# Kernel optimization log

Hardware: AMD Instinct MI355X
Metric: run time of the kernel (lower is better)

The kernel has to match this reference:

```python
import jax, jax.numpy as jnp
import numpy as np
from jax import lax

B, CIN, HW = 4, 3, 256      # batch, image channels, image size
HID = 128                   # hidden_size
EMB_D = 64                  # embedding_dim == encoder output channels
K = 1024                    # num_embeddings
L = 2                       # num encoder/decoder layers (1 resblock each)


def _conv(x, w, b, stride, pad):
    y = lax.conv_general_dilated(x, w, (stride, stride), ((pad, pad), (pad, pad)),
                                 dimension_numbers=('NCHW', 'OIHW', 'NCHW'))
    return y + b[None, :, None, None]


def _bn(x):
    # BatchNorm2d in training mode: batch stats over (N,H,W), affine at init (gamma=1, beta=0)
    m = x.mean((0, 2, 3), keepdims=True)
    v = x.var((0, 2, 3), keepdims=True)
    return (x - m) * lax.rsqrt(v + 1e-5)


def _resblock(x, w1, b1, w2, b2):
    y = jax.nn.relu(_bn(_conv(x, w1, b1, 1, 1)))
    y = _bn(_conv(y, w2, b2, 1, 1))
    return jax.nn.relu(y + x)


def _conv_t(x, w, b):
    # torch ConvTranspose2d(k=4, s=2, p=1); w in torch layout (I, O, 4, 4)
    wf = jnp.flip(w, (2, 3)).transpose(1, 0, 2, 3)  # (O, I, 4, 4)
    y = lax.conv_general_dilated(x, wf, (1, 1), ((2, 2), (2, 2)), lhs_dilation=(2, 2),
                                 dimension_numbers=('NCHW', 'OIHW', 'NCHW'))
    return y + b[None, :, None, None]


def _vqvae(x, enc_in_w, enc_in_b, enc_res_w1, enc_res_b1, enc_res_w2, enc_res_b2,
           enc_down_w, enc_down_b, enc_out_w, enc_out_b,
           dec_in_w, dec_in_b, dec_res_w1, dec_res_b1, dec_res_w2, dec_res_b2,
           dec_up_w, dec_up_b, dec_out_w, dec_out_b, codebook):
    sg = lax.stop_gradient
    # ---- encoder ----
    h = _conv(x, enc_in_w, enc_in_b, 1, 0)
    for i in range(L):
        h = _resblock(h, enc_res_w1[i], enc_res_b1[i], enc_res_w2[i], enc_res_b2[i])
        h = jax.nn.relu(_conv(h, enc_down_w[i], enc_down_b[i], 2, 1))
    z = _conv(h, enc_out_w, enc_out_b, 1, 0)  # (B, C, H/4, W/4)
    # ---- vector quantize ----
    Bz, C, Hl, Wl = z.shape
    zf = z.transpose(0, 2, 3, 1).reshape(-1, C)  # (N, C)
    # ||z - e||^2 expanded; same argmin as the (N,K,C) form without materializing it
    d = (zf * zf).sum(1, keepdims=True) - 2.0 * (zf @ codebook.T) + (codebook * codebook).sum(1)[None, :]
    idx = jnp.argmin(d, axis=1)  # (N,)
    z_q = codebook[idx].reshape(Bz, Hl, Wl, C).transpose(0, 3, 1, 2)
    z_q_st = z_q + sg(z - z_q)  # as in source: forward value == z, grads flow to codebook
    # ---- decoder ----
    h = _conv(z_q_st, dec_in_w, dec_in_b, 1, 0)
    for i in range(L):
        h = _resblock(h, dec_res_w1[i], dec_res_b1[i], dec_res_w2[i], dec_res_b2[i])
        h = jax.nn.relu(_conv_t(h, dec_up_w[i], dec_up_b[i]))
    recon = jax.nn.sigmoid(_conv(h, dec_out_w, dec_out_b, 1, 0))
    # ---- losses ----
    commit = jnp.mean((z - sg(z_q_st)) ** 2)
    cb_l = jnp.mean((sg(z) - z_q_st) ** 2)
    counts = jnp.zeros((K,), jnp.float32).at[idx].add(1.0)
    p = counts + 1e-6
    p = p / p.sum()
    ent = -(p * jnp.log(p)).sum()
    loss = commit + cb_l - ent
    return recon, loss, idx.reshape(Bz, Hl, Wl)


def setup_inputs() -> dict:
    key = jax.random.key(0)
    ks = iter(jax.random.split(key, 40))
    def w(shape, fan_in):
        return jax.random.normal(next(ks), shape, jnp.float32) * np.float32((2.0 / fan_in) ** 0.5)
    z128 = lambda *s: jnp.zeros(s, jnp.float32)
    return {
        'x': jax.random.uniform(next(ks), (B, CIN, HW, HW), jnp.float32),
        'enc_in_w': w((HID, CIN, 1, 1), CIN), 'enc_in_b': z128(HID),
        'enc_res_w1': w((L, HID, HID, 3, 3), HID * 9), 'enc_res_b1': z128(L, HID),
        'enc_res_w2': w((L, HID, HID, 3, 3), HID * 9), 'enc_res_b2': z128(L, HID),
        'enc_down_w': w((L, HID, HID, 4, 4), HID * 16), 'enc_down_b': z128(L, HID),
        'enc_out_w': w((EMB_D, HID, 1, 1), HID), 'enc_out_b': z128(EMB_D),
        'dec_in_w': w((HID, EMB_D, 1, 1), EMB_D), 'dec_in_b': z128(HID),
        'dec_res_w1': w((L, HID, HID, 3, 3), HID * 9), 'dec_res_b1': z128(L, HID),
        'dec_res_w2': w((L, HID, HID, 3, 3), HID * 9), 'dec_res_b2': z128(L, HID),
        'dec_up_w': w((L, HID, HID, 4, 4), HID * 16), 'dec_up_b': z128(L, HID),  # (I,O,4,4) torch layout
        'dec_out_w': w((CIN, HID, 1, 1), HID), 'dec_out_b': z128(CIN),
        'codebook': jax.random.normal(next(ks), (K, EMB_D), jnp.float32) * np.float32((2.0 / (K + EMB_D)) ** 0.5),
    }


def reference(x, enc_in_w, enc_in_b, enc_res_w1, enc_res_b1, enc_res_w2, enc_res_b2,
              enc_down_w, enc_down_b, enc_out_w, enc_out_b,
              dec_in_w, dec_in_b, dec_res_w1, dec_res_b1, dec_res_w2, dec_res_b2,
              dec_up_w, dec_up_b, dec_out_w, dec_out_b, codebook):
    return _vqvae(x, enc_in_w, enc_in_b, enc_res_w1, enc_res_b1, enc_res_w2, enc_res_b2,
                  enc_down_w, enc_down_b, enc_out_w, enc_out_b,
                  dec_in_w, dec_in_b, dec_res_w1, dec_res_b1, dec_res_w2, dec_res_b2,
                  dec_up_w, dec_up_b, dec_out_w, dec_out_b, codebook)
```

## Files before the change

### kernel.cpp

```cpp
#include <hip/hip_runtime.h>
#include <math.h>


#define RE_SIZE 786432

typedef float f32x4 __attribute__((ext_vector_type(4)));
typedef short bf16x8 __attribute__((ext_vector_type(8)));
typedef short bf16x4 __attribute__((ext_vector_type(4)));

__device__ __forceinline__ unsigned short f2bf(float f) {
  unsigned u = __float_as_uint(f);
  return (unsigned short)((u + 0x7fffu + ((u >> 16) & 1u)) >> 16);
}
__device__ __forceinline__ float bf2f(unsigned short h) {
  return __uint_as_float(((unsigned)h) << 16);
}
__device__ __forceinline__ void split3(float v, unsigned short& a,
                                       unsigned short& b, unsigned short& c) {
  a = f2bf(v); float r = v - bf2f(a);
  b = f2bf(r); r -= bf2f(b);
  c = f2bf(r);
}

__global__ __launch_bounds__(256) void weff_kernel(
    const float* __restrict__ w3, const float* __restrict__ ew,
    const float* __restrict__ eb, unsigned short* __restrict__ f0,
    unsigned short* __restrict__ f1, unsigned short* __restrict__ f2) {
  int id = blockIdx.x * 256 + threadIdx.x;
  int j = id & 7, lane = (id >> 3) & 63, mt = (id >> 9) & 7, kc = id >> 12;
  int co = mt * 16 + (lane & 15);
  int q = lane >> 4;
  int k = kc * 32 + q * 8 + j;
  int t = k >> 2, c = k & 3;
  float v = 0.f;
  if (t <= 8) {
    double acc = 0.0;
    for (int ci = 0; ci < 128; ++ci) {
      double wv = (double)w3[((long)co * 128 + ci) * 9 + t];
      double xv = (c < 3) ? (double)ew[ci * 3 + c] : (double)eb[ci];
      acc += wv * xv;
    }
    v = (float)acc;
  }
  unsigned short a, b, cc; split3(v, a, b, cc);
  f0[id] = a; f1[id] = b; f2[id] = cc;
}

__global__ __launch_bounds__(256) void conv36_mfma_kernel(
    const float* __restrict__ xin, const unsigned short* __restrict__ f0,
    const unsigned short* __restrict__ f1, const unsigned short* __restrict__ f2,
    const float* __restrict__ bias, float* __restrict__ out, int H, int W) {
  __shared__ __align__(16) unsigned short s_x[3][720];
  int tid = threadIdx.x, wv = tid >> 6, lane = tid & 63;
  int q = lane >> 4, c15 = lane & 15;
  int tilesX = W >> 4;
  int tx0 = (blockIdx.x % tilesX) << 4;
  int ty0 = (blockIdx.x / tilesX) << 3;
  int n = blockIdx.z;
  long HWl = (long)H * W;
  long ibase = (long)n * 128 * HWl;
  long xbase = (long)n * 3 * HWl;
  f32x4 acc[2][8];
#pragma unroll
  for (int a = 0; a < 2; ++a)
#pragma unroll
    for (int b = 0; b < 8; ++b) acc[a][b] = (f32x4){0.f, 0.f, 0.f, 0.f};

  for (int l = tid; l < 180; l += 256) {
    int y = l / 18, x = l % 18;
    int gy = ty0 + y - 1, gx = tx0 + x - 1;
    float v[4] = {0.f, 0.f, 0.f, 0.f};
    if ((unsigned)gy < (unsigned)H && (unsigned)gx < (unsigned)W) {
      const float* xp = xin + xbase + (long)gy * W + gx;
      v[0] = xp[0]; v[1] = xp[HWl]; v[2] = xp[2 * HWl]; v[3] = 1.f;
    }
    bf16x4 s0, s1, s2;
#pragma unroll
    for (int c = 0; c < 4; ++c) {
      unsigned short h0, h1, h2; split3(v[c], h0, h1, h2);
      s0[c] = (short)h0; s1[c] = (short)h1; s2[c] = (short)h2;
    }
    *(bf16x4*)(s_x[0] + l * 4) = s0;
    *(bf16x4*)(s_x[1] + l * 4) = s1;
    *(bf16x4*)(s_x[2] + l * 4) = s2;
  }
  __syncthreads();

#pragma unroll
  for (int kc = 0; kc < 2; ++kc) {
    bf16x8 a0[2], a1[2], a2[2];
#pragma unroll
// ... 3 lines not shown
      a1[m] = ((const bf16x8*)f1)[fi];
      a2[m] = ((const bf16x8*)f2)[fi];
    }
    int ta = kc * 8 + 2 * q; if (ta > 8) ta = 8;
    int tb = ta + 1;         if (tb > 8) tb = 8;
    int pa_d = (ta / 3) * 18 + ta % 3;
    int pb_d = (tb / 3) * 18 + tb % 3;
#pragma unroll
    for (int nn = 0; nn < 8; ++nn) {
      int pa = (nn * 18 + c15 + pa_d) * 4;
      int pb = (nn * 18 + c15 + pb_d) * 4;
      bf16x8 b0, b1v, b2;
      bf16x4 lo, hi;
      lo = *(const bf16x4*)(s_x[0] + pa); hi = *(const bf16x4*)(s_x[0] + pb);
#pragma unroll
      for (int i = 0; i < 4; ++i) { b0[i] = lo[i]; b0[4 + i] = hi[i]; }
      lo = *(const bf16x4*)(s_x[1] + pa); hi = *(const bf16x4*)(s_x[1] + pb);
#pragma unroll
      for (int i = 0; i < 4; ++i) { b1v[i] = lo[i]; b1v[4 + i] = hi[i]; }
      lo = *(const bf16x4*)(s_x[2] + pa); hi = *(const bf16x4*)(s_x[2] + pb);
#pragma unroll
      for (int i = 0; i < 4; ++i) { b2[i] = lo[i]; b2[4 + i] = hi[i]; }
#pragma unroll
      for (int m = 0; m < 2; ++m) {
        acc[m][nn] = __builtin_amdgcn_mfma_f32_16x16x32_bf16(a0[m], b0, acc[m][nn], 0, 0, 0);
        acc[m][nn] = __builtin_amdgcn_mfma_f32_16x16x32_bf16(a0[m], b1v, acc[m][nn], 0, 0, 0);
        acc[m][nn] = __builtin_amdgcn_mfma_f32_16x16x32_bf16(a1[m], b0, acc[m][nn], 0, 0, 0);
        acc[m][nn] = __builtin_amdgcn_mfma_f32_16x16x32_bf16(a0[m], b2, acc[m][nn], 0, 0, 0);
        acc[m][nn] = __builtin_amdgcn_mfma_f32_16x16x32_bf16(a1[m], b1v, acc[m][nn], 0, 0, 0);
        acc[m][nn] = __builtin_amdgcn_mfma_f32_16x16x32_bf16(a2[m], b0, acc[m][nn], 0, 0, 0);
      }
    }
  }
#pragma unroll
  for (int mt2 = 0; mt2 < 2; ++mt2) {
    int co0 = (wv * 2 + mt2) * 16 + q * 4;
#pragma unroll
    for (int nn = 0; nn < 8; ++nn) {
      long pxoff = ibase + (long)(ty0 + nn) * W + tx0 + c15;
#pragma unroll
      for (int r = 0; r < 4; ++r)
        out[pxoff + (long)(co0 + r) * HWl] = acc[mt2][nn][r] + bias[co0 + r];
    }
  }
}

__global__ __launch_bounds__(256) void wsplit_kernel(
    const float* __restrict__ w, unsigned short* __restrict__ w0,
    unsigned short* __restrict__ w1, unsigned short* __restrict__ w2) {
  int id = blockIdx.x * 256 + threadIdx.x;
  int j = id & 7, lane = (id >> 3) & 63, rest = id >> 9;
  int mt = rest & 7, rest2 = rest >> 3;
  int tap = rest2 % 9, cc = rest2 / 9;
  int co = mt * 16 + (lane & 15);
  int ci = cc * 32 + (lane >> 4) * 8 + j;
  float v = w[((long)co * 128 + ci) * 9 + tap];
  unsigned short a, b, c; split3(v, a, b, c);
  w0[id] = a; w1[id] = b; w2[id] = c;
}

__global__ __launch_bounds__(256) void wsplit4_kernel(
    const float* __restrict__ w, unsigned short* __restrict__ w0,
    unsigned short* __restrict__ w1, unsigned short* __restrict__ w2) {
  int id = blockIdx.x * 256 + threadIdx.x;
  int j = id & 7, lane = (id >> 3) & 63;
  int mt = (id >> 9) & 7, pair = (id >> 12) & 7, cc = id >> 15;
  int q = lane >> 4;
  int tap = pair * 2 + (q >> 1);
  int ky = tap >> 2, kx = tap & 3;
  int co = mt * 16 + (lane & 15);
  int ci = cc * 16 + (q & 1) * 8 + j;
  float v = w[((long)co * 128 + ci) * 16 + ky * 4 + kx];
  unsigned short a, b, c; split3(v, a, b, c);
  w0[id] = a; w1[id] = b; w2[id] = c;
}

__global__ __launch_bounds__(256) void wsplitT_kernel(
    const float* __restrict__ w, unsigned short* __restrict__ w0,
    unsigned short* __restrict__ w1) {
  int id = blockIdx.x * 256 + threadIdx.x;
  int jj = id & 7, lane = (id >> 3) & 63;
  int mt = (id >> 9) & 7, j = (id >> 12) & 3, cls = (id >> 14) & 3, cc = id >> 16;
  int py = cls >> 1, px = cls & 1, jy = j >> 1, jx = j & 1;
  int ky = py ? (jy ? 2 : 0) : (jy ? 3 : 1);
  int kx = px ? (jx ? 2 : 0) : (jx ? 3 : 1);
  int co = mt * 16 + (lane & 15);
  int ci = cc * 32 + (lane >> 4) * 8 + jj;
  float v = w[((long)ci * 128 + co) * 16 + ky * 4 + kx];
  unsigned short h = f2bf(v);
  w0[id] = h;
  w1[id] = f2bf(v - bf2f(h));
}

template<int IMODE, int SPLIT>
__global__ __launch_bounds__(256) void conv3x3_mfma_kernel(
    const float* __restrict__ in, const unsigned short* __restrict__ w0s,
    const unsigned short* __restrict__ w1s, const unsigned short* __restrict__ w2s,
    const float* __restrict__ bias, float* __restrict__ out, int H, int W,
    const float2* __restrict__ mr, const float* __restrict__ xin,
    const float* __restrict__ w1, const float* __restrict__ b1) {
  __shared__ __align__(16) unsigned short s_x[SPLIT][5760];
  int tid = threadIdx.x, wv = tid >> 6, lane = tid & 63;
  int q = lane >> 4, c15 = lane & 15;
  int tilesX = W >> 4;
  int tx0 = (blockIdx.x % tilesX) << 4;
  int ty0 = (blockIdx.x / tilesX) << 3;
  int n = blockIdx.z;
  long HWl = (long)H * W;
  long ibase = (long)n * 128 * HWl;
  f32x4 acc[2][8];
#pragma unroll
  for (int a = 0; a < 2; ++a)
#pragma unroll
    for (int b = 0; b < 8; ++b) acc[a][b] = (f32x4){0.f, 0.f, 0.f, 0.f};

  for (int cc = 0; cc < 4; ++cc) {
    __syncthreads();
    for (int l = tid; l < 720; l += 256) {
      int cig = l / 180, px = l % 180;
      int y = px / 18, x = px % 18;
      int gy = ty0 + y - 1, gx = tx0 + x - 1;
      float v[8];
      if ((unsigned)gy < (unsigned)H && (unsigned)gx < (unsigned)W) {
        if (IMODE == 2) {
          const float* xp = xin + (long)n * 3 * HWl + (long)gy * W + gx;
          float x0 = xp[0], x1 = xp[HWl], x2 = xp[2 * HWl];
#pragma unroll
          for (int c = 0; c < 8; ++c) {
            int ci = cc * 32 + cig * 8 + c;
            v[c] = fmaf(w1[ci * 3 + 0], x0,
                   fmaf(w1[ci * 3 + 1], x1,
                   fmaf(w1[ci * 3 + 2], x2, b1[ci])));
          }
        } else {
          const float* ip = in + ibase + (long)(cc * 32 + cig * 8) * HWl
                            + (long)gy * W + gx;
#pragma unroll
          for (int c = 0; c < 8; ++c) v[c] = ip[(long)c * HWl];
          if (IMODE == 1) {
#pragma unroll
            for (int c = 0; c < 8; ++c) {
              float2 s = mr[cc * 32 + cig * 8 + c];
              v[c] = fmaxf((v[c] - s.x) * s.y, 0.f);
            }
          }
        }
      } else {
#pragma unroll
        for (int c = 0; c < 8; ++c) v[c] = 0.f;
      }
      bf16x8 sv[SPLIT];
#pragma unroll
      for (int c = 0; c < 8; ++c) {
        unsigned short h0 = f2bf(v[c]); float r = v[c] - bf2f(h0);
        unsigned short h1 = f2bf(r);
        sv[0][c] = (short)h0; sv[1][c] = (short)h1;
        if (SPLIT == 3) { r -= bf2f(h1); sv[2][c] = (short)f2bf(r); }
      }
#pragma unroll
      for (int s = 0; s < SPLIT; ++s) *(bf16x8*)(s_x[s] + l * 8) = sv[s];
    }
    __syncthreads();

    for (int tap = 0; tap < 9; ++tap) {
      int dy = tap / 3, dx = tap % 3;
      long fbase = (long)((cc * 9 + tap) * 8) * 64;
      bf16x8 a0[2], a1[2], a2[2];
#pragma unroll
      for (int m = 0; m < 2; ++m) {
        long fi = fbase + (2 * wv + m) * 64 + lane;
        a0[m] = ((const bf16x8*)w0s)[fi];
        a1[m] = ((const bf16x8*)w1s)[fi];
        if (SPLIT == 3) a2[m] = ((const bf16x8*)w2s)[fi];
      }
      int xoff = (q * 180 + dy * 18 + c15 + dx) * 8;
#pragma unroll
      for (int nn = 0; nn < 8; ++nn) {
        bf16x8 b0 = *(const bf16x8*)(s_x[0] + xoff + nn * 144);
        bf16x8 b1v = *(const bf16x8*)(s_x[1] + xoff + nn * 144);
#pragma unroll
        for (int m = 0; m < 2; ++m) {
          acc[m][nn] = __builtin_amdgcn_mfma_f32_16x16x32_bf16(a0[m], b0, acc[m][nn], 0, 0, 0);
          acc[m][nn] = __builtin_amdgcn_mfma_f32_16x16x32_bf16(a0[m], b1v, acc[m][nn], 0, 0, 0);
          acc[m][nn] = __builtin_amdgcn_mfma_f32_16x16x32_bf16(a1[m], b0, acc[m][nn], 0, 0, 0);
        }
        if (SPLIT == 3) {
          bf16x8 b2 = *(const bf16x8*)(s_x[2] + xoff + nn * 144);
#pragma unroll
          for (int m = 0; m < 2; ++m) {
            acc[m][nn] = __builtin_amdgcn_mfma_f32_16x16x32_bf16(a0[m], b2, acc[m][nn], 0, 0, 0);
            acc[m][nn] = __builtin_amdgcn_mfma_f32_16x16x32_bf16(a1[m], b1v, acc[m][nn], 0, 0, 0);
            acc[m][nn] = __builtin_amdgcn_mfma_f32_16x16x32_bf16(a2[m], b0, acc[m][nn], 0, 0, 0);
          }
        }
      }
    }
  }
#pragma unroll
  for (int mt2 = 0; mt2 < 2; ++mt2) {
    int co0 = (wv * 2 + mt2) * 16 + q * 4;
#pragma unroll
    for (int nn = 0; nn < 8; ++nn) {
      long pxoff = ibase + (long)(ty0 + nn) * W + tx0 + c15;
#pragma unroll
      for (int r = 0; r < 4; ++r)
        out[pxoff + (long)(co0 + r) * HWl] = acc[mt2][nn][r] + bias[co0 + r];
    }
  }
}

__global__ __launch_bounds__(256) void down_mfma_kernel(
    const float* __restrict__ in, const unsigned short* __restrict__ w0s,
    const unsigned short* __restrict__ w1s, const unsigned short* __restrict__ w2s,
    const float* __restrict__ bias, float* __restrict__ out, int Hin, int Win) {
  __shared__ __align__(16) unsigned short s_x[3][9792];
  int tid = threadIdx.x, wv = tid >> 6, lane = tid & 63;
  int q = lane >> 4, c15 = lane & 15;
  int Hout = Hin >> 1, Wout = Win >> 1;
  int tilesX = Wout >> 4;
  int tx0 = (blockIdx.x % tilesX) << 4;
  int ty0 = (blockIdx.x / tilesX) << 3;
  int n = blockIdx.z;
  long HWin = (long)Hin * Win, HWout = (long)Hout * Wout;
  long ibase = (long)n * 128 * HWin, obase = (long)n * 128 * HWout;
  f32x4 acc[2][8];
#pragma unroll
  for (int a = 0; a < 2; ++a)
#pragma unroll
    for (int b = 0; b < 8; ++b) acc[a][b] = (f32x4){0.f, 0.f, 0.f, 0.f};

  for (int cc = 0; cc < 8; ++cc) {
    __syncthreads();
    for (int l = tid; l < 1224; l += 256) {
      int cig = l / 612, rem = l % 612;
      int g = rem / 153, p = rem % 153;
      int py = p / 17, px_ = p % 17;
      int gy = g >> 1, gx = g & 1;
      int iy = 2 * (ty0 + py - gy) + gy;
      int ix = 2 * (tx0 + px_ - gx) + gx;
      float v[8];
      if ((unsigned)iy < (unsigned)Hin && (unsigned)ix < (unsigned)Win) {
        const float* ip = in + ibase + (long)(cc * 16 + cig * 8) * HWin
                          + (long)iy * Win + ix;
#pragma unroll
        for (int c = 0; c < 8; ++c) v[c] = ip[(long)c * HWin];
      } else {
#pragma unroll
        for (int c = 0; c < 8; ++c) v[c] = 0.f;
      }
      bf16x8 s0, s1, s2;
#pragma unroll
      for (int c = 0; c < 8; ++c) {
        unsigned short h0, h1, h2; split3(v[c], h0, h1, h2);
        s0[c] = (short)h0; s1[c] = (short)h1; s2[c] = (short)h2;
      }
      *(bf16x8*)(s_x[0] + l * 8) = s0;
      *(bf16x8*)(s_x[1] + l * 8) = s1;
      *(bf16x8*)(s_x[2] + l * 8) = s2;
    }
    __syncthreads();

    for (int pr = 0; pr < 8; ++pr) {
      long fbase = (long)((cc * 8 + pr) * 8) * 64;
      bf16x8 a0[2], a1[2], a2[2];
#pragma unroll
      for (int m = 0; m < 2; ++m) {
        long fi = fbase + (2 * wv + m) * 64 + lane;
        a0[m] = ((const bf16x8*)w0s)[fi];
        a1[m] = ((const bf16x8*)w1s)[fi];
        a2[m] = ((const bf16x8*)w2s)[fi];
      }
      int tap = pr * 2 + (q >> 1);
      int ky = tap >> 2, kx = tap & 3;
      int gy = (ky + 1) & 1, gx = (kx + 1) & 1;
      int dy = (ky == 0) ? -1 : ((ky == 3) ? 1 : 0);
      int dx = (kx == 0) ? -1 : ((kx == 3) ? 1 : 0);
      int g = gy * 2 + gx, cig = q & 1;
      int xoff = ((cig * 4 + g) * 153 + (dy + gy) * 17 + (c15 + dx + gx)) * 8;
#pragma unroll
      for (int nn = 0; nn < 8; ++nn) {
        bf16x8 b0 = *(const bf16x8*)(s_x[0] + xoff + nn * 136);
        bf16x8 b1v = *(const bf16x8*)(s_x[1] + xoff + nn * 136);
        bf16x8 b2 = *(const bf16x8*)(s_x[2] + xoff + nn * 136);
#pragma unroll
        for (int m = 0; m < 2; ++m) {
          acc[m][nn] = __builtin_amdgcn_mfma_f32_16x16x32_bf16(a0[m], b0, acc[m][nn], 0, 0, 0);
          acc[m][nn] = __builtin_amdgcn_mfma_f32_16x16x32_bf16(a0[m], b1v, acc[m][nn], 0, 0, 0);
          acc[m][nn] = __builtin_amdgcn_mfma_f32_16x16x32_bf16(a1[m], b0, acc[m][nn], 0, 0, 0);
          acc[m][nn] = __builtin_amdgcn_mfma_f32_16x16x32_bf16(a0[m], b2, acc[m][nn], 0, 0, 0);
          acc[m][nn] = __builtin_amdgcn_mfma_f32_16x16x32_bf16(a1[m], b1v, acc[m][nn], 0, 0, 0);
          acc[m][nn] = __builtin_amdgcn_mfma_f32_16x16x32_bf16(a2[m], b0, acc[m][nn], 0, 0, 0);
        }
      }
    }
  }
#pragma unroll
  for (int mt2 = 0; mt2 < 2; ++mt2) {
    int co0 = (wv * 2 + mt2) * 16 + q * 4;
#pragma unroll
    for (int nn = 0; nn < 8; ++nn) {
      long pxoff = obase + (long)(ty0 + nn) * Wout + tx0 + c15;
#pragma unroll
      for (int r = 0; r < 4; ++r)
        out[pxoff + (long)(co0 + r) * HWout] =
            fmaxf(acc[mt2][nn][r] + bias[co0 + r], 0.f);
    }
  }
}

__global__ __launch_bounds__(256) void up_mfma_kernel(
    const float* __restrict__ in, const unsigned short* __restrict__ wh,
    const unsigned short* __restrict__ wl, const float* __restrict__ bias,
    float* __restrict__ out, int Hin, int Win) {
  __shared__ __align__(16) unsigned short s_xh[5760];
  __shared__ __align__(16) unsigned short s_xl[5760];
  int tid = threadIdx.x, wv = tid >> 6, lane = tid & 63;
  int q = lane >> 4, c15 = lane & 15;
  int cls = blockIdx.z & 3, n = blockIdx.z >> 2;
  int py = cls >> 1, px = cls & 1;
  int Hout = Hin << 1, Wout = Win << 1;
  int tilesX = Win >> 4;
  int x0 = (blockIdx.x % tilesX) << 4;
  int m0 = (blockIdx.x / tilesX) << 3;
  long HWin = (long)Hin * Win, HWout = (long)Hout * Wout;
  long ibase = (long)n * 128 * HWin, obase = (long)n * 128 * HWout;
  f32x4 acc[2][8];
#pragma unroll
  for (int a = 0; a < 2; ++a)
#pragma unroll
    for (int b = 0; b < 8; ++b) acc[a][b] = (f32x4){0.f, 0.f, 0.f, 0.f};

  for (int cc = 0; cc < 4; ++cc) {
    __syncthreads();
    for (int l = tid; l < 720; l += 256) {
      int cig = l / 180, p = l % 180;
      int y = p / 18, x = p % 18;
      int gy = m0 + y - 1, gx = x0 + x - 1;
      float v[8];
      if ((unsigned)gy < (unsigned)Hin && (unsigned)gx < (unsigned)Win) {
        const float* ip = in + ibase + (long)(cc * 32 + cig * 8) * HWin
                          + (long)gy * Win + gx;
#pragma unroll
        for (int c = 0; c < 8; ++c) v[c] = ip[(long)c * HWin];
      } else {
#pragma unroll
        for (int c = 0; c < 8; ++c) v[c] = 0.f;
      }
      bf16x8 hv, lv;
#pragma unroll
      for (int c = 0; c < 8; ++c) {
        unsigned short h = f2bf(v[c]);
        hv[c] = (short)h;
        lv[c] = (short)f2bf(v[c] - bf2f(h));
      }
      *(bf16x8*)(s_xh + l * 8) = hv;
      *(bf16x8*)(s_xl + l * 8) = lv;
    }
    __syncthreads();

#pragma unroll
    for (int j = 0; j < 4; ++j) {
      int jy = j >> 1, jx = j & 1;
      int dy = py ? (jy ? 0 : 1) : (jy ? -1 : 0);
      int dx = px ? (jx ? 0 : 1) : (jx ? -1 : 0);
      long fbase = (long)((((cc * 4 + cls) * 4 + j) * 8)) * 64;
      const bf16x8* aph = (const bf16x8*)wh + fbase;
      const bf16x8* apl = (const bf16x8*)wl + fbase;
      bf16x8 ah0 = aph[(2 * wv) * 64 + lane];
      bf16x8 ah1 = aph[(2 * wv + 1) * 64 + lane];
      bf16x8 al0 = apl[(2 * wv) * 64 + lane];
      bf16x8 al1 = apl[(2 * wv + 1) * 64 + lane];
      int xoff = (q * 180 + (dy + 1) * 18 + (c15 + dx + 1)) * 8;
#pragma unroll
      for (int nn = 0; nn < 8; ++nn) {
        bf16x8 bh = *(const bf16x8*)(s_xh + xoff + nn * 144);
        bf16x8 bl = *(const bf16x8*)(s_xl + xoff + nn * 144);
// ... 33 lines not shown
  int HW4 = HW >> 2;
  long p4 = (long)blockIdx.x * blockDim.x + threadIdx.x;
  if (p4 >= (long)N * HW4) return;
  int n = (int)(p4 / HW4), hw4 = (int)(p4 % HW4);
  const float4* inp = (const float4*)(in + (long)n * Cin * HW) + hw4;
  float4* outp = (float4*)(out + (long)n * Cout * HW) + hw4;
  float4 acc[CW];
#pragma unroll
  for (int j = 0; j < CW; ++j) { float bb = bias[co0 + j]; acc[j] = make_float4(bb, bb, bb, bb); }
  for (int ci = 0; ci < Cin; ++ci) {
    float4 v = inp[(long)ci * HW4];
#pragma unroll
    for (int j = 0; j < CW; ++j) {
      float ww = wl[j * Cin + ci];
      acc[j].x = fmaf(ww, v.x, acc[j].x);
      acc[j].y = fmaf(ww, v.y, acc[j].y);
      acc[j].z = fmaf(ww, v.z, acc[j].z);
      acc[j].w = fmaf(ww, v.w, acc[j].w);
    }
  }
#pragma unroll
  for (int j = 0; j < CW; ++j) {
    float4 v = acc[j];
    if (ACT == 2) {
      v.x = 1.f / (1.f + expf(-v.x));
      v.y = 1.f / (1.f + expf(-v.y));
      v.z = 1.f / (1.f + expf(-v.z));
      v.w = 1.f / (1.f + expf(-v.w));
    }
    outp[(long)(co0 + j) * HW4] = v;
  }
}

__global__ __launch_bounds__(256) void bn_part_kernel(
    const float* __restrict__ x, float2* __restrict__ part, int HW) {
  int c = blockIdx.x, sl = blockIdx.y, tid = threadIdx.x;
  int seg = HW >> 3;
  double s = 0.0, ss = 0.0;
  for (int n = 0; n < 4; ++n) {
    const float4* xp = (const float4*)(x + ((long)(n * 128 + c)) * HW + (long)sl * seg);
    for (int i = tid; i < (seg >> 2); i += 256) {
      float4 v = xp[i];
      s  += (double)v.x + (double)v.y + (double)v.z + (double)v.w;
      ss += (double)v.x * v.x + (double)v.y * v.y + (double)v.z * v.z + (double)v.w * v.w;
    }
  }
  __shared__ double shs[256], shss[256];
  shs[tid] = s; shss[tid] = ss;
  __syncthreads();
  for (int off = 128; off > 0; off >>= 1) {
    if (tid < off) { shs[tid] += shs[tid + off]; shss[tid] += shss[tid + off]; }
    __syncthreads();
  }
  if (tid == 0) part[c * 8 + sl] = make_float2((float)shs[0], (float)shss[0]);
}

__global__ __launch_bounds__(128) void bn_final_kernel(
    const float2* __restrict__ part, float2* __restrict__ mr, float cntf) {
  int c = threadIdx.x;
  if (c < 128) {
    double s = 0.0, ss = 0.0;
#pragma unroll
    for (int i = 0; i < 8; ++i) { float2 p = part[c * 8 + i]; s += p.x; ss += p.y; }
    double cnt = (double)cntf;
    double m = s / cnt;
    double var = ss / cnt - m * m;
    mr[c] = make_float2((float)m, (float)(1.0 / sqrt(var + 1e-5)));
  }
}

template<int RMODE>
__global__ __launch_bounds__(256) void bn_res_relu_kernel(
    float* __restrict__ y, const float2* __restrict__ mr,
    const float* __restrict__ res,
    const float* __restrict__ xin, const float* __restrict__ w1,
    const float* __restrict__ b1, int HW4) {
  int nc = blockIdx.y;
  int c = nc & 127, n = nc >> 7;
  float2 s = mr[c];
  int i = blockIdx.x * blockDim.x + threadIdx.x;
  if (i >= HW4) return;
  long off = (long)nc * HW4 + i;
  float4 v = ((const float4*)y)[off];
  v.x = (v.x - s.x) * s.y; v.y = (v.y - s.x) * s.y;
  v.z = (v.z - s.x) * s.y; v.w = (v.w - s.x) * s.y;
  float4 r4;
  if (RMODE == 0) {
    r4 = ((const float4*)res)[off];
  } else {
    const float4* xp = (const float4*)(xin) + (long)n * 3 * HW4 + i;
    float4 x0 = xp[0], x1 = xp[HW4], x2 = xp[2 * HW4];
    float wa = w1[c * 3 + 0], wb = w1[c * 3 + 1], wc = w1[c * 3 + 2], bb = b1[c];
    r4.x = fmaf(wa, x0.x, fmaf(wb, x1.x, fmaf(wc, x2.x, bb)));
    r4.y = fmaf(wa, x0.y, fmaf(wb, x1.y, fmaf(wc, x2.y, bb)));
    r4.z = fmaf(wa, x0.z, fmaf(wb, x1.z, fmaf(wc, x2.z, bb)));
    r4.w = fmaf(wa, x0.w, fmaf(wb, x1.w, fmaf(wc, x2.w, bb)));
  }
  v.x = fmaxf(v.x + r4.x, 0.f); v.y = fmaxf(v.y + r4.y, 0.f);
  v.z = fmaxf(v.z + r4.z, 0.f); v.w = fmaxf(v.w + r4.w, 0.f);
  ((float4*)y)[off] = v;
}

__global__ __launch_bounds__(256) void vq_kernel(
    const float* __restrict__ z, const float* __restrict__ cb,
    float* __restrict__ idx_out, float* __restrict__ counts, int HWl) {
  __shared__ float s_z[64][65];
  __shared__ float s_cb[64][64];
  __shared__ float s_bd[4][64];
  __shared__ int   s_bk[4][64];
  int tid = threadIdx.x;
  int r0 = blockIdx.x * 64;
  for (int l = tid; l < 64 * 64; l += 256) {
    int c = l >> 6, rs = l & 63;
    int r = r0 + rs;
    int n = r / HWl, rem = r % HWl;
    s_z[rs][c] = z[((long)(n * 64 + c)) * HWl + rem];
  }
  int row = tid & 63, cg = tid >> 6;
  float best = 3.4e38f; int bestk = 0;
  for (int k0 = 0; k0 < 1024; k0 += 64) {
    __syncthreads();
    for (int l = tid; l < 4096; l += 256)
      s_cb[l >> 6][l & 63] = cb[(long)(k0 + (l >> 6)) * 64 + (l & 63)];
    __syncthreads();
#pragma unroll
    for (int j = 0; j < 16; ++j) {
      int kk = cg * 16 + j;
      const float* zp = s_z[row];
      const float* cp = s_cb[kk];
      float d = 0.f;
#pragma unroll
      for (int c = 0; c < 64; ++c) {
// ... 53 lines not shown
                              void* d_out, int out_size, void* d_ws, size_t ws_size,
                              hipStream_t stream) {
  (void)in_sizes; (void)n_in; (void)out_size; (void)ws_size;
  const float* x          = (const float*)d_in[0];
  const float* enc_in_w   = (const float*)d_in[1];
  const float* enc_in_b   = (const float*)d_in[2];
  const float* enc_res_w1 = (const float*)d_in[3];
  const float* enc_res_b1 = (const float*)d_in[4];
  const float* enc_res_w2 = (const float*)d_in[5];
  const float* enc_res_b2 = (const float*)d_in[6];
  const float* enc_down_w = (const float*)d_in[7];
  const float* enc_down_b = (const float*)d_in[8];
  const float* enc_out_w  = (const float*)d_in[9];
  const float* enc_out_b  = (const float*)d_in[10];
  const float* dec_in_w   = (const float*)d_in[11];
  const float* dec_in_b   = (const float*)d_in[12];
  const float* dec_res_w1 = (const float*)d_in[13];
  const float* dec_res_b1 = (const float*)d_in[14];
  const float* dec_res_w2 = (const float*)d_in[15];
  const float* dec_res_b2 = (const float*)d_in[16];
  const float* dec_up_w   = (const float*)d_in[17];
  const float* dec_up_b   = (const float*)d_in[18];
  const float* dec_out_w  = (const float*)d_in[19];
  const float* dec_out_b  = (const float*)d_in[20];
  const float* codebook   = (const float*)d_in[21];
  float* out = (float*)d_out;

  const long BIG = 33554432;
  const long S1 = 8388608, S2 = 16777216, S3 = 25165824;
  float* P0 = (float*)d_ws;
  float* P1 = P0 + BIG;
  float2* mr   = (float2*)out;
  float* hist  = out + 256;
  float2* part = (float2*)(out + 1280);
  unsigned short* W0 = (unsigned short*)(out + 4096);
  unsigned short* W1 = (unsigned short*)(out + 135168);
  unsigned short* W2 = (unsigned short*)(out + 266240);
  unsigned short* F0 = (unsigned short*)(out + 401408);
  unsigned short* F1 = F0 + 8192;
  unsigned short* F2 = F1 + 8192;

  const int W3 = 128 * 128 * 9, W4 = 128 * 128 * 16, BS = 128;
  const dim3 g256(512, 1, 4), g128(128, 1, 4), g64(32, 1, 4);

  weff_kernel<<<32, 256, 0, stream>>>(enc_res_w1, enc_in_w, enc_in_b, F0, F1, F2);
  conv36_mfma_kernel<<<g256, 256, 0, stream>>>(
      x, F0, F1, F2, enc_res_b1, P0, 256, 256);
  bn_part_kernel<<<dim3(128, 8), 256, 0, stream>>>(P0, part, 65536);
  bn_final_kernel<<<1, 128, 0, stream>>>(part, mr, 262144.f);
  wsplit_kernel<<<576, 256, 0, stream>>>(enc_res_w2, W0, W1, W2);
  conv3x3_mfma_kernel<1, 3><<<g256, 256, 0, stream>>>(
      P0, W0, W1, W2, enc_res_b2, P1, 256, 256, mr, nullptr, nullptr, nullptr);
  bn_part_kernel<<<dim3(128, 8), 256, 0, stream>>>(P1, part, 65536);
  bn_final_kernel<<<1, 128, 0, stream>>>(part, mr, 262144.f);
  bn_res_relu_kernel<1><<<dim3(64, 512), 256, 0, stream>>>(
      P1, mr, nullptr, x, enc_in_w, enc_in_b, 16384);
  wsplit4_kernel<<<1024, 256, 0, stream>>>(enc_down_w, W0, W1, W2);
  down_mfma_kernel<<<g128, 256, 0, stream>>>(P1, W0, W1, W2, enc_down_b, P0, 256, 256);

  wsplit_kernel<<<576, 256, 0, stream>>>(enc_res_w1 + W3, W0, W1, W2);
  conv3x3_mfma_kernel<0, 3><<<g128, 256, 0, stream>>>(
      P0, W0, W1, W2, enc_res_b1 + BS, P0 + S1, 128, 128, nullptr, nullptr, nullptr, nullptr);
  bn_part_kernel<<<dim3(128, 8), 256, 0, stream>>>(P0 + S1, part, 16384);
  bn_final_kernel<<<1, 128, 0, stream>>>(part, mr, 65536.f);
  wsplit_kernel<<<576, 256, 0, stream>>>(enc_res_w2 + W3, W0, W1, W2);
  conv3x3_mfma_kernel<1, 3><<<g128, 256, 0, stream>>>(
      P0 + S1, W0, W1, W2, enc_res_b2 + BS, P0 + S2, 128, 128, mr, nullptr, nullptr, nullptr);
  bn_part_kernel<<<dim3(128, 8), 256, 0, stream>>>(P0 + S2, part, 16384);
  bn_final_kernel<<<1, 128, 0, stream>>>(part, mr, 65536.f);
  bn_res_relu_kernel<0><<<dim3(16, 512), 256, 0, stream>>>(
      P0 + S2, mr, P0, nullptr, nullptr, nullptr, 4096);
  wsplit4_kernel<<<1024, 256, 0, stream>>>(enc_down_w + W4, W0, W1, W2);
  down_mfma_kernel<<<g64, 256, 0, stream>>>(P0 + S2, W0, W1, W2, enc_down_b + BS, P0 + S3, 128, 128);

  conv1x1_kernel<0, 16><<<dim3(16, 4), 256, 16 * 128 * 4, stream>>>(
      P0 + S3, enc_out_w, enc_out_b, P1, 4, 128, 64, 4096);

  zero_kernel<<<4, 256, 0, stream>>>(hist, 1024);
  vq_kernel<<<256, 256, 0, stream>>>(P1, codebook, out + RE_SIZE + 1, hist, 4096);
  entropy_kernel<<<1, 256, 0, stream>>>(hist, out + RE_SIZE);

  conv1x1_kernel<0, 16><<<dim3(16, 8), 256, 16 * 64 * 4, stream>>>(
      P1, dec_in_w, dec_in_b, P0, 4, 64, 128, 4096);

  wsplit_kernel<<<576, 256, 0, stream>>>(dec_res_w1, W0, W1, W2);
  conv3x3_mfma_kernel<0, 2><<<g64, 256, 0, stream>>>(
      P0, W0, W1, W2, dec_res_b1, P0 + S1, 64, 64, nullptr, nullptr, nullptr, nullptr);
  bn_part_kernel<<<dim3(128, 8), 256, 0, stream>>>(P0 + S1, part, 4096);
  bn_final_kernel<<<1, 128, 0, stream>>>(part, mr, 16384.f);
  wsplit_kernel<<<576, 256, 0, stream>>>(dec_res_w2, W0, W1, W2);
  conv3x3_mfma_kernel<1, 2><<<g64, 256, 0, stream>>>(
      P0 + S1, W0, W1, W2, dec_res_b2, P0 + S2, 64, 64, mr, nullptr, nullptr, nullptr);
  bn_part_kernel<<<dim3(128, 8), 256, 0, stream>>>(P0 + S2, part, 4096);
  bn_final_kernel<<<1, 128, 0, stream>>>(part, mr, 16384.f);
  bn_res_relu_kernel<0><<<dim3(4, 512), 256, 0, stream>>>(
      P0 + S2, mr, P0, nullptr, nullptr, nullptr, 1024);
  wsplitT_kernel<<<1024, 256, 0, stream>>>(dec_up_w, W0, W1);
  up_mfma_kernel<<<dim3(32, 1, 16), 256, 0, stream>>>(
      P0 + S2, W0, W1, dec_up_b, P0 + S3, 64, 64);

  wsplit_kernel<<<576, 256, 0, stream>>>(dec_res_w1 + W3, W0, W1, W2);
  conv3x3_mfma_kernel<0, 2><<<g128, 256, 0, stream>>>(
      P0 + S3, W0, W1, W2, dec_res_b1 + BS, P1, 128, 128, nullptr, nullptr, nullptr, nullptr);
  bn_part_kernel<<<dim3(128, 8), 256, 0, stream>>>(P1, part, 16384);
  bn_final_kernel<<<1, 128, 0, stream>>>(part, mr, 65536.f);
  wsplit_kernel<<<576, 256, 0, stream>>>(dec_res_w2 + W3, W0, W1, W2);
  conv3x3_mfma_kernel<1, 2><<<g128, 256, 0, stream>>>(
      P1, W0, W1, W2, dec_res_b2 + BS, P1 + S1, 128, 128, mr, nullptr, nullptr, nullptr);
  bn_part_kernel<<<dim3(128, 8), 256, 0, stream>>>(P1 + S1, part, 16384);
  bn_final_kernel<<<1, 128, 0, stream>>>(part, mr, 65536.f);
  bn_res_relu_kernel<0><<<dim3(16, 512), 256, 0, stream>>>(
      P1 + S1, mr, P0 + S3, nullptr, nullptr, nullptr, 4096);
  wsplitT_kernel<<<1024, 256, 0, stream>>>(dec_up_w + W4, W0, W1);
  up_mfma_kernel<<<dim3(128, 1, 16), 256, 0, stream>>>(
      P1 + S1, W0, W1, dec_up_b + BS, P0, 128, 128);

  conv1x1_kernel<2, 3><<<dim3(256, 1), 256, 3 * 128 * 4, stream>>>(
      P0, dec_out_w, dec_out_b, out, 4, 128, 3, 65536);
}
```

Before: 1.651 ms.

## Fuse BN statistics into conv epilogues and BN-residual-ReLU into consumer loads

Each conv kernel now accumulates per-channel sum and sum-of-squares in double while it writes its output, reduces them across lanes with shuffles, and atomically adds them into sliced partial buffers. This removes the separate bn_part reduction passes over every conv output. Most bn_res_relu passes are folded into the input staging of the following down or up conv, which normalises, adds the residual and applies ReLU on the fly. That saves a full read-modify-write of large activations, at the cost of double-precision atomics, extra residual reads inside the conv loads, and a zeroing of partials inside bn_final.

```diff
diff --git a/kernel.cpp b/kernel.cpp
--- a/kernel.cpp
+++ b/kernel.cpp
@@ -21,6 +21,38 @@
   b = f2bf(r); r -= bf2f(b);
   c = f2bf(r);
 }
+
+#define CONV_EPILOGUE_STATS(OUTBASE, ROWSTRIDE, CHSTRIDE)                      \
+  {                                                                            \
+    double sA[2][4], qA[2][4];                                                 \
+    _Pragma("unroll") for (int a = 0; a < 2; ++a)                              \
+      _Pragma("unroll") for (int r = 0; r < 4; ++r) { sA[a][r] = 0.0; qA[a][r] = 0.0; } \
+    _Pragma("unroll") for (int mt2 = 0; mt2 < 2; ++mt2) {                      \
+      int co0 = (wv * 2 + mt2) * 16 + q * 4;                                   \
+      _Pragma("unroll") for (int nn = 0; nn < 8; ++nn) {                       \
+        long pxoff = (OUTBASE) + (long)nn * (ROWSTRIDE);                       \
+        _Pragma("unroll") for (int r = 0; r < 4; ++r) {                        \
+          float v = acc[mt2][nn][r] + bias[co0 + r];                           \
+          out[pxoff + (long)(co0 + r) * (CHSTRIDE)] = v;                       \
+          sA[mt2][r] += (double)v; qA[mt2][r] += (double)v * (double)v;        \
+        }                                                                      \
+      }                                                                        \
+    }                                                                          \
+    _Pragma("unroll") for (int m = 1; m < 16; m <<= 1)                         \
+      _Pragma("unroll") for (int a = 0; a < 2; ++a)                            \
+        _Pragma("unroll") for (int r = 0; r < 4; ++r) {                        \
+          sA[a][r] += __shfl_xor(sA[a][r], m);                                 \
+          qA[a][r] += __shfl_xor(qA[a][r], m);                                 \
+        }                                                                      \
+    if (c15 == 0) {                                                            \
+      _Pragma("unroll") for (int a = 0; a < 2; ++a)                            \
+        _Pragma("unroll") for (int r = 0; r < 4; ++r) {                        \
+          int co = (wv * 2 + a) * 16 + q * 4 + r;                              \
+          atomicAdd(&part[(slice * 128 + co) * 2 + 0], sA[a][r]);              \
+          atomicAdd(&part[(slice * 128 + co) * 2 + 1], qA[a][r]);              \
+        }                                                                      \
+    }                                                                          \
+  }
 
 __global__ __launch_bounds__(256) void weff_kernel(
     const float* __restrict__ w3, const float* __restrict__ ew,
@@ -49,7 +81,8 @@
 __global__ __launch_bounds__(256) void conv36_mfma_kernel(
     const float* __restrict__ xin, const unsigned short* __restrict__ f0,
     const unsigned short* __restrict__ f1, const unsigned short* __restrict__ f2,
-    const float* __restrict__ bias, float* __restrict__ out, int H, int W) {
+    const float* __restrict__ bias, float* __restrict__ out,
+    double* __restrict__ part, int H, int W) {
   __shared__ __align__(16) unsigned short s_x[3][720];
   int tid = threadIdx.x, wv = tid >> 6, lane = tid & 63;
   int q = lane >> 4, c15 = lane & 15;
@@ -57,6 +90,7 @@
   int tx0 = (blockIdx.x % tilesX) << 4;
   int ty0 = (blockIdx.x / tilesX) << 3;
   int n = blockIdx.z;
+  int slice = blockIdx.x & 7;
   long HWl = (long)H * W;
   long ibase = (long)n * 128 * HWl;
   long xbase = (long)n * 3 * HWl;
@@ -126,17 +160,8 @@
       }
     }
   }
-#pragma unroll
-  for (int mt2 = 0; mt2 < 2; ++mt2) {
-    int co0 = (wv * 2 + mt2) * 16 + q * 4;
-#pragma unroll
-    for (int nn = 0; nn < 8; ++nn) {
-      long pxoff = ibase + (long)(ty0 + nn) * W + tx0 + c15;
-#pragma unroll
-      for (int r = 0; r < 4; ++r)
-        out[pxoff + (long)(co0 + r) * HWl] = acc[mt2][nn][r] + bias[co0 + r];
-    }
-  }
+  long ob = ibase + (long)ty0 * W + tx0 + c15;
+  CONV_EPILOGUE_STATS(ob, W, HWl)
 }
 
 __global__ __launch_bounds__(256) void wsplit_kernel(
@@ -191,8 +216,7 @@
     const float* __restrict__ in, const unsigned short* __restrict__ w0s,
     const unsigned short* __restrict__ w1s, const unsigned short* __restrict__ w2s,
     const float* __restrict__ bias, float* __restrict__ out, int H, int W,
-    const float2* __restrict__ mr, const float* __restrict__ xin,
-    const float* __restrict__ w1, const float* __restrict__ b1) {
+    const float2* __restrict__ mr, double* __restrict__ part) {
   __shared__ __align__(16) unsigned short s_x[SPLIT][5760];
   int tid = threadIdx.x, wv = tid >> 6, lane = tid & 63;
   int q = lane >> 4, c15 = lane & 15;
@@ -200,6 +224,7 @@
   int tx0 = (blockIdx.x % tilesX) << 4;
   int ty0 = (blockIdx.x / tilesX) << 3;
   int n = blockIdx.z;
+  int slice = blockIdx.x & 7;
   long HWl = (long)H * W;
   long ibase = (long)n * 128 * HWl;
   f32x4 acc[2][8];
@@ -216,27 +241,15 @@
       int gy = ty0 + y - 1, gx = tx0 + x - 1;
       float v[8];
       if ((unsigned)gy < (unsigned)H && (unsigned)gx < (unsigned)W) {
-        if (IMODE == 2) {
-          const float* xp = xin + (long)n * 3 * HWl + (long)gy * W + gx;
-          float x0 = xp[0], x1 = xp[HWl], x2 = xp[2 * HWl];
+        const float* ip = in + ibase + (long)(cc * 32 + cig * 8) * HWl
+                          + (long)gy * W + gx;
+#pragma unroll
+        for (int c = 0; c < 8; ++c) v[c] = ip[(long)c * HWl];
+        if (IMODE == 1) {
 #pragma unroll
           for (int c = 0; c < 8; ++c) {
-            int ci = cc * 32 + cig * 8 + c;
-            v[c] = fmaf(w1[ci * 3 + 0], x0,
-                   fmaf(w1[ci * 3 + 1], x1,
-                   fmaf(w1[ci * 3 + 2], x2, b1[ci])));
-          }
-        } else {
-          const float* ip = in + ibase + (long)(cc * 32 + cig * 8) * HWl
-                            + (long)gy * W + gx;
-#pragma unroll
-          for (int c = 0; c < 8; ++c) v[c] = ip[(long)c * HWl];
-          if (IMODE == 1) {
-#pragma unroll
-            for (int c = 0; c < 8; ++c) {
-              float2 s = mr[cc * 32 + cig * 8 + c];
-              v[c] = fmaxf((v[c] - s.x) * s.y, 0.f);
-            }
+            float2 s = mr[cc * 32 + cig * 8 + c];
+            v[c] = fmaxf((v[c] - s.x) * s.y, 0.f);
           }
         }
       } else {
@@ -290,23 +303,18 @@
       }
     }
   }
-#pragma unroll
-  for (int mt2 = 0; mt2 < 2; ++mt2) {
-    int co0 = (wv * 2 + mt2) * 16 + q * 4;
-#pragma unroll
-    for (int nn = 0; nn < 8; ++nn) {
-      long pxoff = ibase + (long)(ty0 + nn) * W + tx0 + c15;
-#pragma unroll
-      for (int r = 0; r < 4; ++r)
-        out[pxoff + (long)(co0 + r) * HWl] = acc[mt2][nn][r] + bias[co0 + r];
-    }
-  }
-}
-
+  long ob = ibase + (long)ty0 * W + tx0 + c15;
+  CONV_EPILOGUE_STATS(ob, W, HWl)
+}
+
+template<int IMODE>
 __global__ __launch_bounds__(256) void down_mfma_kernel(
     const float* __restrict__ in, const unsigned short* __restrict__ w0s,
     const unsigned short* __restrict__ w1s, const unsigned short* __restrict__ w2s,
-    const float* __restrict__ bias, float* __restrict__ out, int Hin, int Win) {
+    const float* __restrict__ bias, float* __restrict__ out, int Hin, int Win,
+    const float2* __restrict__ mr, const float* __restrict__ res,
+    const float* __restrict__ xin, const float* __restrict__ ew,
+    const float* __restrict__ eb) {
   __shared__ __align__(16) unsigned short s_x[3][9792];
   int tid = threadIdx.x, wv = tid >> 6, lane = tid & 63;
   int q = lane >> 4, c15 = lane & 15;
@@ -334,10 +342,29 @@
       int ix = 2 * (tx0 + px_ - gx) + gx;
       float v[8];
       if ((unsigned)iy < (unsigned)Hin && (unsigned)ix < (unsigned)Win) {
-        const float* ip = in + ibase + (long)(cc * 16 + cig * 8) * HWin
-                          + (long)iy * Win + ix;
+        int cb0 = cc * 16 + cig * 8;
+        const float* ip = in + ibase + (long)cb0 * HWin + (long)iy * Win + ix;
 #pragma unroll
         for (int c = 0; c < 8; ++c) v[c] = ip[(long)c * HWin];
+        float x0 = 0.f, x1 = 0.f, x2 = 0.f;
+        if (IMODE == 2) {
+          const float* xp = xin + (long)n * 3 * HWin + (long)iy * Win + ix;
+          x0 = xp[0]; x1 = xp[HWin]; x2 = xp[2 * HWin];
+        }
+        const float* rp = (IMODE == 1)
+            ? res + ibase + (long)cb0 * HWin + (long)iy * Win + ix : nullptr;
+#pragma unroll
+        for (int c = 0; c < 8; ++c) {
+          float2 s = mr[cb0 + c];
+          float rv;
+          if (IMODE == 1) rv = rp[(long)c * HWin];
+          else {
+            int ci = cb0 + c;
+            rv = fmaf(ew[ci * 3 + 0], x0, fmaf(ew[ci * 3 + 1], x1,
+                 fmaf(ew[ci * 3 + 2], x2, eb[ci])));
+          }
+          v[c] = fmaxf((v[c] - s.x) * s.y + rv, 0.f);
+        }
       } else {
 #pragma unroll
         for (int c = 0; c < 8; ++c) v[c] = 0.f;
@@ -402,10 +429,12 @@
   }
 }
 
+template<int UMODE>
 __global__ __launch_bounds__(256) void up_mfma_kernel(
     const float* __restrict__ in, const unsigned short* __restrict__ wh,
     const unsigned short* __restrict__ wl, const float* __restrict__ bias,
-    float* __restrict__ out, int Hin, int Win) {
+    float* __restrict__ out, int Hin, int Win,
+    const float2* __restrict__ mr, const float* __restrict__ res) {
   __shared__ __align__(16) unsigned short s_xh[5760];
   __shared__ __align__(16) unsigned short s_xl[5760];
   int tid = threadIdx.x, wv = tid >> 6, lane = tid & 63;
@@ -432,10 +461,18 @@
       int gy = m0 + y - 1, gx = x0 + x - 1;
       float v[8];
       if ((unsigned)gy < (unsigned)Hin && (unsigned)gx < (unsigned)Win) {
-        const float* ip = in + ibase + (long)(cc * 32 + cig * 8) * HWin
-                          + (long)gy * Win + gx;
+        int cb0 = cc * 32 + cig * 8;
+        const float* ip = in + ibase + (long)cb0 * HWin + (long)gy * Win + gx;
 #pragma unroll
         for (int c = 0; c < 8; ++c) v[c] = ip[(long)c * HWin];
+        if (UMODE == 1) {
+          const float* rp = res + ibase + (long)cb0 * HWin + (long)gy * Win + gx;
+#pragma unroll
+          for (int c = 0; c < 8; ++c) {
+            float2 s = mr[cb0 + c];
+            v[c] = fmaxf((v[c] - s.x) * s.y + rp[(long)c * HWin], 0.f);
+          }
+        }
       } else {
 #pragma unroll
         for (int c = 0; c < 8; ++c) v[c] = 0.f;
@@ -535,72 +572,41 @@
   }
 }
 
-__global__ __launch_bounds__(256) void bn_part_kernel(
-    const float* __restrict__ x, float2* __restrict__ part, int HW) {
-  int c = blockIdx.x, sl = blockIdx.y, tid = threadIdx.x;
-  int seg = HW >> 3;
+__global__ __launch_bounds__(128) void bn_final_kernel(
+    double* __restrict__ part, float2* __restrict__ mr, float cntf) {
+  int c = threadIdx.x;
   double s = 0.0, ss = 0.0;
-  for (int n = 0; n < 4; ++n) {
-    const float4* xp = (const float4*)(x + ((long)(n * 128 + c)) * HW + (long)sl * seg);
-    for (int i = tid; i < (seg >> 2); i += 256) {
-      float4 v = xp[i];
-      s  += (double)v.x + (double)v.y + (double)v.z + (double)v.w;
-      ss += (double)v.x * v.x + (double)v.y * v.y + (double)v.z * v.z + (double)v.w * v.w;
-    }
-  }
-  __shared__ double shs[256], shss[256];
-  shs[tid] = s; shss[tid] = ss;
-  __syncthreads();
-  for (int off = 128; off > 0; off >>= 1) {
-    if (tid < off) { shs[tid] += shs[tid + off]; shss[tid] += shss[tid + off]; }
-    __syncthreads();
-  }
-  if (tid == 0) part[c * 8 + sl] = make_float2((float)shs[0], (float)shss[0]);
-}
-
-__global__ __launch_bounds__(128) void bn_final_kernel(
-    const float2* __restrict__ part, float2* __restrict__ mr, float cntf) {
-  int c = threadIdx.x;
-  if (c < 128) {
-    double s = 0.0, ss = 0.0;
-#pragma unroll
-    for (int i = 0; i < 8; ++i) { float2 p = part[c * 8 + i]; s += p.x; ss += p.y; }
-    double cnt = (double)cntf;
-    double m = s / cnt;
-    double var = ss / cnt - m * m;
-    mr[c] = make_float2((float)m, (float)(1.0 / sqrt(var + 1e-5)));
-  }
-}
-
-template<int RMODE>
+#pragma unroll
+  for (int sl = 0; sl < 8; ++sl) {
+    s  += part[(sl * 128 + c) * 2 + 0];
+    ss += part[(sl * 128 + c) * 2 + 1];
+  }
+  double cnt = (double)cntf;
+  double m = s / cnt;
+  double var = ss / cnt - m * m;
+  mr[c] = make_float2((float)m, (float)(1.0 / sqrt(var + 1e-5)));
+#pragma unroll
+  for (int sl = 0; sl < 8; ++sl) {
+    part[(sl * 128 + c) * 2 + 0] = 0.0;
+    part[(sl * 128 + c) * 2 + 1] = 0.0;
+  }
+}
+
 __global__ __launch_bounds__(256) void bn_res_relu_kernel(
     float* __restrict__ y, const float2* __restrict__ mr,
-    const float* __restrict__ res,
-    const float* __restrict__ xin, const float* __restrict__ w1,
-    const float* __restrict__ b1, int HW4) {
+    const float* __restrict__ res, int HW4) {
   int nc = blockIdx.y;
-  int c = nc & 127, n = nc >> 7;
+  int c = nc & 127;
   float2 s = mr[c];
   int i = blockIdx.x * blockDim.x + threadIdx.x;
   if (i >= HW4) return;
   long off = (long)nc * HW4 + i;
   float4 v = ((const float4*)y)[off];
-  v.x = (v.x - s.x) * s.y; v.y = (v.y - s.x) * s.y;
-  v.z = (v.z - s.x) * s.y; v.w = (v.w - s.x) * s.y;
-  float4 r4;
-  if (RMODE == 0) {
-    r4 = ((const float4*)res)[off];
-  } else {
-    const float4* xp = (const float4*)(xin) + (long)n * 3 * HW4 + i;
-    float4 x0 = xp[0], x1 = xp[HW4], x2 = xp[2 * HW4];
-    float wa = w1[c * 3 + 0], wb = w1[c * 3 + 1], wc = w1[c * 3 + 2], bb = b1[c];
-    r4.x = fmaf(wa, x0.x, fmaf(wb, x1.x, fmaf(wc, x2.x, bb)));
-    r4.y = fmaf(wa, x0.y, fmaf(wb, x1.y, fmaf(wc, x2.y, bb)));
-    r4.z = fmaf(wa, x0.z, fmaf(wb, x1.z, fmaf(wc, x2.z, bb)));
-    r4.w = fmaf(wa, x0.w, fmaf(wb, x1.w, fmaf(wc, x2.w, bb)));
-  }
-  v.x = fmaxf(v.x + r4.x, 0.f); v.y = fmaxf(v.y + r4.y, 0.f);
-  v.z = fmaxf(v.z + r4.z, 0.f); v.w = fmaxf(v.w + r4.w, 0.f);
+  float4 r4 = ((const float4*)res)[off];
+  v.x = fmaxf((v.x - s.x) * s.y + r4.x, 0.f);
+  v.y = fmaxf((v.y - s.x) * s.y + r4.y, 0.f);
+  v.z = fmaxf((v.z - s.x) * s.y + r4.z, 0.f);
+  v.w = fmaxf((v.w - s.x) * s.y + r4.w, 0.f);
   ((float4*)y)[off] = v;
 }
 
@@ -720,10 +726,10 @@
   float* P1 = P0 + BIG;
   float2* mr   = (float2*)out;
   float* hist  = out + 256;
-  float2* part = (float2*)(out + 1280);
-  unsigned short* W0 = (unsigned short*)(out + 4096);
-  unsigned short* W1 = (unsigned short*)(out + 135168);
-  unsigned short* W2 = (unsigned short*)(out + 266240);
+  double* part = (double*)(out + 1280);
+  unsigned short* W0 = (unsigned short*)(out + 8192);
+  unsigned short* W1 = (unsigned short*)(out + 139264);
+  unsigned short* W2 = (unsigned short*)(out + 270336);
   unsigned short* F0 = (unsigned short*)(out + 401408);
   unsigned short* F1 = F0 + 8192;
   unsigned short* F2 = F1 + 8192;
@@ -731,40 +737,36 @@
   const int W3 = 128 * 128 * 9, W4 = 128 * 128 * 16, BS = 128;
   const dim3 g256(512, 1, 4), g128(128, 1, 4), g64(32, 1, 4);
 
+  zero_kernel<<<20, 256, 0, stream>>>(out + 256, 5120);
+
   weff_kernel<<<32, 256, 0, stream>>>(enc_res_w1, enc_in_w, enc_in_b, F0, F1, F2);
   conv36_mfma_kernel<<<g256, 256, 0, stream>>>(
-      x, F0, F1, F2, enc_res_b1, P0, 256, 256);
-  bn_part_kernel<<<dim3(128, 8), 256, 0, stream>>>(P0, part, 65536);
+      x, F0, F1, F2, enc_res_b1, P0, part, 256, 256);
   bn_final_kernel<<<1, 128, 0, stream>>>(part, mr, 262144.f);
   wsplit_kernel<<<576, 256, 0, stream>>>(enc_res_w2, W0, W1, W2);
   conv3x3_mfma_kernel<1, 3><<<g256, 256, 0, stream>>>(
-      P0, W0, W1, W2, enc_res_b2, P1, 256, 256, mr, nullptr, nullptr, nullptr);
-  bn_part_kernel<<<dim3(128, 8), 256, 0, stream>>>(P1, part, 65536);
+      P0, W0, W1, W2, enc_res_b2, P1, 256, 256, mr, part);
   bn_final_kernel<<<1, 128, 0, stream>>>(part, mr, 262144.f);
-  bn_res_relu_kernel<1><<<dim3(64, 512), 256, 0, stream>>>(
-      P1, mr, nullptr, x, enc_in_w, enc_in_b, 16384);
   wsplit4_kernel<<<1024, 256, 0, stream>>>(enc_down_w, W0, W1, W2);
-  down_mfma_kernel<<<g128, 256, 0, stream>>>(P1, W0, W1, W2, enc_down_b, P0, 256, 256);
+  down_mfma_kernel<2><<<g128, 256, 0, stream>>>(
+      P1, W0, W1, W2, enc_down_b, P0, 256, 256, mr, nullptr, x, enc_in_w, enc_in_b);
 
   wsplit_kernel<<<576, 256, 0, stream>>>(enc_res_w1 + W3, W0, W1, W2);
   conv3x3_mfma_kernel<0, 3><<<g128, 256, 0, stream>>>(
-      P0, W0, W1, W2, enc_res_b1 + BS, P0 + S1, 128, 128, nullptr, nullptr, nullptr, nullptr);
-  bn_part_kernel<<<dim3(128, 8), 256, 0, stream>>>(P0 + S1, part, 16384);
+      P0, W0, W1, W2, enc_res_b1 + BS, P0 + S1, 128, 128, nullptr, part);
   bn_final_kernel<<<1, 128, 0, stream>>>(part, mr, 65536.f);
   wsplit_kernel<<<576, 256, 0, stream>>>(enc_res_w2 + W3, W0, W1, W2);
   conv3x3_mfma_kernel<1, 3><<<g128, 256, 0, stream>>>(
-      P0 + S1, W0, W1, W2, enc_res_b2 + BS, P0 + S2, 128, 128, mr, nullptr, nullptr, nullptr);
-  bn_part_kernel<<<dim3(128, 8), 256, 0, stream>>>(P0 + S2, part, 16384);
+      P0 + S1, W0, W1, W2, enc_res_b2 + BS, P0 + S2, 128, 128, mr, part);
   bn_final_kernel<<<1, 128, 0, stream>>>(part, mr, 65536.f);
-  bn_res_relu_kernel<0><<<dim3(16, 512), 256, 0, stream>>>(
-      P0 + S2, mr, P0, nullptr, nullptr, nullptr, 4096);
   wsplit4_kernel<<<1024, 256, 0, stream>>>(enc_down_w + W4, W0, W1, W2);
-  down_mfma_kernel<<<g64, 256, 0, stream>>>(P0 + S2, W0, W1, W2, enc_down_b + BS, P0 + S3, 128, 128);
+  down_mfma_kernel<1><<<g64, 256, 0, stream>>>(
+      P0 + S2, W0, W1, W2, enc_down_b + BS, P0 + S3, 128, 128, mr, P0,
+      nullptr, nullptr, nullptr);
 
   conv1x1_kernel<0, 16><<<dim3(16, 4), 256, 16 * 128 * 4, stream>>>(
       P0 + S3, enc_out_w, enc_out_b, P1, 4, 128, 64, 4096);
 
-  zero_kernel<<<4, 256, 0, stream>>>(hist, 1024);
   vq_kernel<<<256, 256, 0, stream>>>(P1, codebook, out + RE_SIZE + 1, hist, 4096);
   entropy_kernel<<<1, 256, 0, stream>>>(hist, out + RE_SIZE);
 
@@ -773,35 +775,29 @@
 
   wsplit_kernel<<<576, 256, 0, stream>>>(dec_res_w1, W0, W1, W2);
   conv3x3_mfma_kernel<0, 2><<<g64, 256, 0, stream>>>(
-      P0, W0, W1, W2, dec_res_b1, P0 + S1, 64, 64, nullptr, nullptr, nullptr, nullptr);
-  bn_part_kernel<<<dim3(128, 8), 256, 0, stream>>>(P0 + S1, part, 4096);
+      P0, W0, W1, W2, dec_res_b1, P0 + S1, 64, 64, nullptr, part);
   bn_final_kernel<<<1, 128, 0, stream>>>(part, mr, 16384.f);
   wsplit_kernel<<<576, 256, 0, stream>>>(dec_res_w2, W0, W1, W2);
   conv3x3_mfma_kernel<1, 2><<<g64, 256, 0, stream>>>(
-      P0 + S1, W0, W1, W2, dec_res_b2, P0 + S2, 64, 64, mr, nullptr, nullptr, nullptr);
-  bn_part_kernel<<<dim3(128, 8), 256, 0, stream>>>(P0 + S2, part, 4096);
+      P0 + S1, W0, W1, W2, dec_res_b2, P0 + S2, 64, 64, mr, part);
   bn_final_kernel<<<1, 128, 0, stream>>>(part, mr, 16384.f);
-  bn_res_relu_kernel<0><<<dim3(4, 512), 256, 0, stream>>>(
-      P0 + S2, mr, P0, nullptr, nullptr, nullptr, 1024);
   wsplitT_kernel<<<1024, 256, 0, stream>>>(dec_up_w, W0, W1);
-  up_mfma_kernel<<<dim3(32, 1, 16), 256, 0, stream>>>(
-      P0 + S2, W0, W1, dec_up_b, P0 + S3, 64, 64);
+  up_mfma_kernel<1><<<dim3(32, 1, 16), 256, 0, stream>>>(
+      P0 + S2, W0, W1, dec_up_b, P0 + S3, 64, 64, mr, P0);
 
   wsplit_kernel<<<576, 256, 0, stream>>>(dec_res_w1 + W3, W0, W1, W2);
   conv3x3_mfma_kernel<0, 2><<<g128, 256, 0, stream>>>(
-      P0 + S3, W0, W1, W2, dec_res_b1 + BS, P1, 128, 128, nullptr, nullptr, nullptr, nullptr);
-  bn_part_kernel<<<dim3(128, 8), 256, 0, stream>>>(P1, part, 16384);
+      P0 + S3, W0, W1, W2, dec_res_b1 + BS, P1, 128, 128, nullptr, part);
   bn_final_kernel<<<1, 128, 0, stream>>>(part, mr, 65536.f);
   wsplit_kernel<<<576, 256, 0, stream>>>(dec_res_w2 + W3, W0, W1, W2);
   conv3x3_mfma_kernel<1, 2><<<g128, 256, 0, stream>>>(
-      P1, W0, W1, W2, dec_res_b2 + BS, P1 + S1, 128, 128, mr, nullptr, nullptr, nullptr);
-  bn_part_kernel<<<dim3(128, 8), 256, 0, stream>>>(P1 + S1, part, 16384);
+      P1, W0, W1, W2, dec_res_b2 + BS, P1 + S1, 128, 128, mr, part);
   bn_final_kernel<<<1, 128, 0, stream>>>(part, mr, 65536.f);
-  bn_res_relu_kernel<0><<<dim3(16, 512), 256, 0, stream>>>(
-      P1 + S1, mr, P0 + S3, nullptr, nullptr, nullptr, 4096);
+  bn_res_relu_kernel<<<dim3(16, 512), 256, 0, stream>>>(
+      P1 + S1, mr, P0 + S3, 4096);
   wsplitT_kernel<<<1024, 256, 0, stream>>>(dec_up_w + W4, W0, W1);
-  up_mfma_kernel<<<dim3(128, 1, 16), 256, 0, stream>>>(
-      P1 + S1, W0, W1, dec_up_b + BS, P0, 128, 128);
+  up_mfma_kernel<0><<<dim3(128, 1, 16), 256, 0, stream>>>(
+      P1 + S1, W0, W1, dec_up_b + BS, P0, 128, 128, nullptr, nullptr);
 
   conv1x1_kernel<2, 3><<<dim3(256, 1), 256, 3 * 128 * 4, stream>>>(
       P0, dec_out_w, dec_out_b, out, 4, 128, 3, 65536);
```

Result: slower. 1.693 ms (+2.6%).
